# Kernel optimization log

Hardware: AMD Instinct MI355X
Metric: run time of the kernel (lower is better)

Reference implementation:

```python
import jax, jax.numpy as jnp
import numpy as np

B, Z, A, H = 2048, 64, 8, 512

def setup_inputs() -> dict:
    key = jax.random.key(0)
    ks = jax.random.split(key, 7)
    s = 1.0 / np.sqrt(H).astype(np.float32)
    z = jax.random.normal(ks[0], (B, Z), jnp.float32)
    # PyTorch LSTM params, gate order [i, f, g, o]
    W_ih = jax.random.uniform(ks[1], (4 * H, A + Z), jnp.float32, -s, s)
    W_hh = jax.random.uniform(ks[2], (4 * H, H), jnp.float32, -s, s)
    b_ih = jax.random.uniform(ks[3], (4 * H,), jnp.float32, -s, s)
    b_hh = jax.random.uniform(ks[4], (4 * H,), jnp.float32, -s, s)
    W_out = jax.random.uniform(ks[5], (A, H), jnp.float32, -s, s)
    b_out = jax.random.uniform(ks[6], (A,), jnp.float32, -s, s)
    return {"z": z, "W_ih": W_ih, "W_hh": W_hh, "b_ih": b_ih, "b_hh": b_hh,
            "W_out": W_out, "b_out": b_out, "seq_len": 64}


def reference(z, W_ih, W_hh, b_ih, b_hh, W_out, b_out, seq_len):
    batch = z.shape[0]
    hidden = W_hh.shape[1]
    act = W_out.shape[0]
    # dec_in_t = [zeros_a, z] is identical at every timestep -> hoist input proj
    dec_in = jnp.concatenate([jnp.zeros((batch, act), z.dtype), z], axis=-1)
    x_proj = dec_in @ W_ih.T + b_ih + b_hh  # (B, 4H), constant per step

    def step(carry, _):
        h, c = carry
        gates = x_proj + h @ W_hh.T  # (B, 4H)
        i, f, g, o = jnp.split(gates, 4, axis=-1)
        i = jax.nn.sigmoid(i)
        f = jax.nn.sigmoid(f)
        g = jnp.tanh(g)
        o = jax.nn.sigmoid(o)
        c = f * c + i * g
        h = o * jnp.tanh(c)
        return (h, c), h

    init = (jnp.zeros((batch, hidden), z.dtype), jnp.zeros((batch, hidden), z.dtype))
    _, hs = jax.lax.scan(step, init, None, length=seq_len)  # (T, B, H)
    hs = jnp.transpose(hs, (1, 0, 2))  # (B, T, H)
    return hs @ W_out.T + b_out  # (B, T, A)
```

## Files before the change

kernel.cpp:

```cpp
#include <hip/hip_runtime.h>


#define HID   512
#define TSTEP 64
#define KCAT  576

typedef __attribute__((ext_vector_type(8))) short bf16x8;
typedef __attribute__((ext_vector_type(4))) float f32x4;

__device__ inline unsigned short f2bf(float f) {
  unsigned int u = __builtin_bit_cast(unsigned int, f);
  unsigned int r = (u + 0x7fffu + ((u >> 16) & 1u)) >> 16;
  return (unsigned short)r;
}
__device__ inline float sigm(float x) { return 1.0f / (1.0f + __expf(-x)); }
__device__ inline float tanh_f(float x) { return 1.0f - 2.0f / (__expf(2.0f * x) + 1.0f); }

__device__ inline void gl16(const unsigned short* g, unsigned short* l) {
  __builtin_amdgcn_global_load_lds(
      (const __attribute__((address_space(1))) unsigned int*)g,
      (__attribute__((address_space(3))) unsigned int*)l, 16, 0, 0);
}

__global__ void k_prep(const float* __restrict__ z, const float* __restrict__ wih,
                       const float* __restrict__ whh, const float* __restrict__ bih,
                       const float* __restrict__ bhh,
                       unsigned short* __restrict__ wcat, unsigned short* __restrict__ zbf,
                       float* __restrict__ bias) {
  int c = blockIdx.x * 256 + threadIdx.x;
  if (c < 147456) {
    int n = c / 72, kc = (c % 72) * 8;
    unsigned short u[8];
#pragma unroll
    for (int e = 0; e < 8; ++e) {
      int k = kc + e;
      float v = (k < 512) ? whh[(size_t)n * 512 + k] : wih[(size_t)n * 72 + 8 + (k - 512)];
      u[e] = f2bf(v);
    }
    *(bf16x8*)&wcat[(size_t)n * KCAT + kc] = *(bf16x8*)u;
  } else if (c < 163840) {
    int i = c - 147456;
    int row = i >> 3, kc = (i & 7) * 8;
    unsigned short u[8];
#pragma unroll
    for (int e = 0; e < 8; ++e) u[e] = f2bf(z[(size_t)row * 64 + kc + e]);
    *(bf16x8*)&zbf[(size_t)row * 64 + kc] = *(bf16x8*)u;
  } else if (c < 165888) {
    int n = c - 163840;
    bias[n] = bih[n] + bhh[n];
  }
}

template <int GATES, int PROJ>
__global__ __launch_bounds__(256, 2) void k_step(
    const unsigned short* __restrict__ hprev, unsigned short* __restrict__ hnext,
    const unsigned short* __restrict__ wcat, const unsigned short* __restrict__ zbf,
    const float* __restrict__ wout, const float* __restrict__ bias,
    const float* __restrict__ bout, float* __restrict__ cst,
    float* __restrict__ out, int t) {
  __shared__ unsigned short Ab[2][64 * 64];
  __shared__ unsigned short Bb[2][128 * 64];
  __shared__ unsigned short wo_lds[16 * 512];
  __shared__ unsigned short hO[64 * 40];

  const int bid = blockIdx.x;
  const int nt = GATES ? (((bid & 7) << 1) | ((bid >> 8) & 1)) : 0;
  const int bt = GATES ? ((bid >> 3) & 31) : bid;
  const int tid = threadIdx.x;
  const int lane = tid & 63;
  const int wv = tid >> 6;
  const int mq = wv >> 1, nh = wv & 1;
  const int cl = lane & 15, q8 = lane >> 4;
  const int b0 = bt * 64, j0 = nt * 32;

  const int rA = tid >> 3;
  const int xA = ((tid & 7) ^ (rA & 7)) * 8;
  const unsigned short* srcA0 = hprev + (size_t)(b0 + rA) * HID + xA;
  const unsigned short* srcA1 = hprev + (size_t)(b0 + 32 + rA) * HID + xA;
  const unsigned short* srcZ0 = zbf + (size_t)(b0 + rA) * 64 + xA;
  const unsigned short* srcZ1 = zbf + (size_t)(b0 + 32 + rA) * 64 + xA;
  const unsigned short* srcB[4];
#pragma unroll
  for (int k = 0; k < 4; ++k) {
    int rB = k * 32 + rA;
    int n = (rB >> 5) * HID + j0 + (rB & 31);
    srcB[k] = wcat + (size_t)n * KCAT + xA;
  }

  auto do_stage = [&](int buf, int kkv) {
    if (GATES) {
      if (kkv == 8) {
        gl16(srcZ0, &Ab[buf][(wv * 64) * 8]);
        gl16(srcZ1, &Ab[buf][(256 + wv * 64) * 8]);
      } else {
        gl16(srcA0 + kkv * 64, &Ab[buf][(wv * 64) * 8]);
        gl16(srcA1 + kkv * 64, &Ab[buf][(256 + wv * 64) * 8]);
      }
#pragma unroll
      for (int k = 0; k < 4; ++k)
        gl16(srcB[k] + kkv * 64, &Bb[buf][(k * 256 + wv * 64) * 8]);
    } else {
      gl16(srcA0 + kkv * 64, &Ab[buf][(wv * 64) * 8]);
      gl16(srcA1 + kkv * 64, &Ab[buf][(256 + wv * 64) * 8]);
    }
  };

  if (PROJ) {
    int r = tid >> 4, s0 = tid & 15;
#pragma unroll
    for (int i = 0; i < 4; ++i) {
      int s = s0 + i * 16;
      unsigned short u[8] = {0, 0, 0, 0, 0, 0, 0, 0};
      if (r < 8) {
        const float* wp = wout + (size_t)r * 512 + s * 8;
        float4 f0 = *(const float4*)wp;
        float4 f1 = *(const float4*)(wp + 4);
        u[0] = f2bf(f0.x); u[1] = f2bf(f0.y); u[2] = f2bf(f0.z); u[3] = f2bf(f0.w);
        u[4] = f2bf(f1.x); u[5] = f2bf(f1.y); u[6] = f2bf(f1.z); u[7] = f2bf(f1.w);
      }
      int off = r * 512 + (s >> 3) * 64 + (((s & 7) ^ (r & 7)) * 8);
      *(bf16x8*)&wo_lds[off] = *(bf16x8*)u;
    }
  }

  f32x4 acc[4][2];
  if (GATES) {
#pragma unroll
    for (int g = 0; g < 4; ++g) {
      float bv = bias[g * HID + j0 + nh * 16 + cl];
      f32x4 v = {bv, bv, bv, bv};
      acc[g][0] = v; acc[g][1] = v;
    }
  }
  f32x4 accp0 = {0, 0, 0, 0}, accp1 = {0, 0, 0, 0};
  if (PROJ) {
    float bo = (cl < 8) ? bout[cl] : 0.0f;
    f32x4 v = {bo, bo, bo, bo};
    accp0 = v; accp1 = v;
  }

  const size_t cbase = ((size_t)bid * 256 + tid) * 8;
  f32x4 c0 = {0, 0, 0, 0}, c1 = {0, 0, 0, 0};
  if (GATES && t > 0) { c0 = *(const f32x4*)&cst[cbase]; c1 = *(const f32x4*)&cst[cbase + 4]; }

  auto mfma_block = [&](int bu, int kkv) {
    const unsigned short* Al = Ab[bu];
    const unsigned short* Bl = Bb[bu];
#pragma unroll
    for (int ks = 0; ks < 2; ++ks) {
      const int sx = ((ks * 4 + q8) ^ (cl & 7)) * 8;
      bf16x8 af0 = *(const bf16x8*)&Al[(mq * 32 + cl) * 64 + sx];
      bf16x8 af1 = *(const bf16x8*)&Al[(mq * 32 + 16 + cl) * 64 + sx];
      if (GATES) {
#pragma unroll
        for (int g = 0; g < 4; ++g) {
          bf16x8 bf = *(const bf16x8*)&Bl[(g * 32 + nh * 16 + cl) * 64 + sx];
          acc[g][0] = __builtin_amdgcn_mfma_f32_16x16x32_bf16(af0, bf, acc[g][0], 0, 0, 0);
          acc[g][1] = __builtin_amdgcn_mfma_f32_16x16x32_bf16(af1, bf, acc[g][1], 0, 0, 0);
        }
      }
      if (PROJ && nh == 0 && kkv < 8) {
        bf16x8 wf = *(const bf16x8*)&wo_lds[cl * 512 + kkv * 64 + sx];
        accp0 = __builtin_amdgcn_mfma_f32_16x16x32_bf16(af0, wf, accp0, 0, 0, 0);
        accp1 = __builtin_amdgcn_mfma_f32_16x16x32_bf16(af1, wf, accp1, 0, 0, 0);
      }
    }
  };

#define MEMBAR() asm volatile("" ::: "memory")
#define HWBAR()  __builtin_amdgcn_s_barrier()

  if (GATES && t == 0) {
    do_stage(0, 8);
    asm volatile("s_waitcnt vmcnt(0) lgkmcnt(0)" ::: "memory");
    HWBAR(); MEMBAR();
    mfma_block(0, 8);
  } else {
    do_stage(0, 0);
    do_stage(1, 1);
    if (GATES) asm volatile("s_waitcnt vmcnt(6) lgkmcnt(0)" ::: "memory");
    else       asm volatile("s_waitcnt vmcnt(2) lgkmcnt(0)" ::: "memory");
    HWBAR(); MEMBAR();
    const int kkEnd = GATES ? 8 : 7;
    for (int kk = 0;; ++kk) {
      mfma_block(kk & 1, kk);
      if (kk == kkEnd) break;
      MEMBAR(); HWBAR(); MEMBAR();
      if (kk + 2 <= kkEnd) {
        do_stage(kk & 1, kk + 2);
        if (GATES) asm volatile("s_waitcnt vmcnt(6)" ::: "memory");
        else       asm volatile("s_waitcnt vmcnt(2)" ::: "memory");
      } else {
        asm volatile("s_waitcnt vmcnt(0)" ::: "memory");
      }
      MEMBAR(); HWBAR(); MEMBAR();
    }
  }

  if (PROJ && nh == 0 && cl < 8) {
    const int tt = t - 1;
#pragma unroll
    for (int r = 0; r < 4; ++r) {
      int b = b0 + mq * 32 + q8 * 4 + r;
      out[((size_t)b * 64 + tt) * 8 + cl] = accp0[r];
      out[((size_t)(b + 16) * 64 + tt) * 8 + cl] = accp1[r];
    }
  }

  if (GATES) {
#pragma unroll
    for (int fm = 0; fm < 2; ++fm) {
      f32x4 cold = fm ? c1 : c0;
      f32x4 cn;
#pragma unroll
      for (int r = 0; r < 4; ++r) {
        float iv = sigm(acc[0][fm][r]);
        float fv = sigm(acc[1][fm][r]);
        float gv = tanh_f(acc[2][fm][r]);
        float ov = sigm(acc[3][fm][r]);
        float cv = fv * cold[r] + iv * gv;
        cn[r] = cv;
        hO[(mq * 32 + fm * 16 + q8 * 4 + r) * 40 + nh * 16 + cl] = f2bf(ov * tanh_f(cv));
      }
      if (fm) c1 = cn; else c0 = cn;
    }
    *(f32x4*)&cst[cbase] = c0;
    *(f32x4*)&cst[cbase + 4] = c1;
    __syncthreads();

    int row = tid >> 2, sg4 = tid & 3;
    unsigned short tmp[8];
#pragma unroll
    for (int e = 0; e < 8; ++e) tmp[e] = hO[row * 40 + sg4 * 8 + e];
    *(int4*)&hnext[(size_t)(b0 + row) * HID + j0 + sg4 * 8] = *(int4*)tmp;
  }
#undef MEMBAR
#undef HWBAR
}

extern "C" void kernel_launch(void* const* d_in, const int* in_sizes, int n_in,
                              void* d_out, int out_size, void* d_ws, size_t ws_size,
                              hipStream_t stream) {
  const float* z    = (const float*)d_in[0];
  const float* wih  = (const float*)d_in[1];
  const float* whh  = (const float*)d_in[2];
  const float* bih  = (const float*)d_in[3];
  const float* bhh  = (const float*)d_in[4];
  const float* wout = (const float*)d_in[5];
  const float* bout = (const float*)d_in[6];
  float* out = (float*)d_out;

  char* ws = (char*)d_ws;
  unsigned short* wcat = (unsigned short*)(ws);
  unsigned short* zbf  = (unsigned short*)(ws + 2359296);
  float* bias          = (float*)(ws + 2621440);
  unsigned short* h0   = (unsigned short*)(ws + 2629632);
  unsigned short* h1   = (unsigned short*)(ws + 4726784);
  float* cst           = (float*)(ws + 6823936);

  k_prep<<<dim3(648), dim3(256), 0, stream>>>(z, wih, whh, bih, bhh, wcat, zbf, bias);

  for (int t = 0; t < TSTEP; ++t) {
    const unsigned short* hp = (t & 1) ? h0 : h1;
    unsigned short* hn = (t & 1) ? h1 : h0;
    if (t == 0)
      k_step<1, 0><<<dim3(512), dim3(256), 0, stream>>>(hp, hn, wcat, zbf, wout, bias,
                                                        bout, cst, out, t);
    else
      k_step<1, 1><<<dim3(512), dim3(256), 0, stream>>>(hp, hn, wcat, zbf, wout, bias,
                                                        bout, cst, out, t);
  }
  k_step<0, 1><<<dim3(32), dim3(256), 0, stream>>>(h1, h0, wcat, zbf, wout, bias,
                                                   bout, cst, out, TSTEP);
}
```

Baseline: 926.7 us.

## Replace per-timestep launches with persistent cooperative kernel using flag-based sync

Replaces the 65 per-timestep kernel launches with one cooperative persistent kernel of 512 blocks. Each block keeps its cell state in registers across steps, keeps the z tile and W_out in LDS, and waits on per-batch-tile counters in global memory before reading the previous h. The aim is to remove launch overhead and the c-state round-trip through global memory. The cost is spin-wait latency and a reliance on all 512 blocks being co-resident; if the cooperative launch fails, the old multi-launch path runs instead.

```diff
diff --git a/kernel.cpp b/kernel.cpp
--- a/kernel.cpp
+++ b/kernel.cpp
@@ -5,6 +5,7 @@
 #define TSTEP 64
 #define KCAT  576
 
+typedef unsigned long long u64;
 typedef __attribute__((ext_vector_type(8))) short bf16x8;
 typedef __attribute__((ext_vector_type(4))) float f32x4;
 
@@ -51,8 +52,269 @@
   }
 }
 
+__global__ void k_zero(int* __restrict__ flags) {
+  int g = blockIdx.x * 256 + threadIdx.x;
+  if (g < TSTEP * 32) flags[g] = 0;
+}
+
+struct P {
+  const unsigned short *wcat, *zbf;
+  const float *bias, *wout, *bout;
+  unsigned short *h0, *h1;
+  float* out;
+  int* flags;
+};
+
+#define ATOMLD(PTR) __hip_atomic_load((PTR), __ATOMIC_RELAXED, __HIP_MEMORY_SCOPE_AGENT)
+#define ATOMST(PTR, V) __hip_atomic_store((PTR), (V), __ATOMIC_RELAXED, __HIP_MEMORY_SCOPE_AGENT)
+
+#define SMEM_SZ 78848
+
+__global__ __launch_bounds__(256, 2) void k_persist(P p) {
+  extern __shared__ char smem[];
+  unsigned short* Bb[2] = {(unsigned short*)smem, (unsigned short*)(smem + 16384)};
+  unsigned short* Ab[2] = {(unsigned short*)(smem + 32768), (unsigned short*)(smem + 40960)};
+  unsigned short* zA    = (unsigned short*)(smem + 49152);
+  unsigned short* wo    = (unsigned short*)(smem + 57344);
+  unsigned short* hO    = (unsigned short*)(smem + 73728);
+
+  const int bid = blockIdx.x;
+  const int nt = bid >> 5, bt = bid & 31;
+  const int tid = threadIdx.x;
+  const int lane = tid & 63;
+  const int wv = tid >> 6;
+  const int mq = wv >> 1, nh = wv & 1;
+  const int cl = lane & 15, q8 = lane >> 4;
+  const int b0 = bt * 64, j0 = nt * 32;
+
+  const int rS = tid >> 3;
+  const int xS = ((tid & 7) ^ (rS & 7)) * 8;
+  const unsigned short* srcB[4];
+#pragma unroll
+  for (int k = 0; k < 4; ++k) {
+    int rB = k * 32 + rS;
+    int n = (rB >> 5) * HID + j0 + (rB & 31);
+    srcB[k] = p.wcat + (size_t)n * KCAT + xS;
+  }
+#define STAGEB(BUF, CHUNK) { _Pragma("unroll") for (int k4 = 0; k4 < 4; ++k4) \
+    gl16(srcB[k4] + (CHUNK) * 64, &Bb[BUF][(k4 * 256 + wv * 64) * 8]); }
+
+  const int arow = tid >> 2, aseg = tid & 3;
+  const int aoff0 = arow * 64 + (((aseg * 2 + 0) ^ (arow & 7)) * 8);
+  const int aoff1 = arow * 64 + (((aseg * 2 + 1) ^ (arow & 7)) * 8);
+#define AWRITE(DST, R) do { \
+    *(u64*)&(DST)[aoff0] = (R)[0]; *(u64*)&(DST)[aoff0 + 4] = (R)[1]; \
+    *(u64*)&(DST)[aoff1] = (R)[2]; *(u64*)&(DST)[aoff1 + 4] = (R)[3]; } while (0)
+
+  {
+    const u64* zp = (const u64*)(p.zbf + (size_t)(b0 + arow) * 64) + aseg * 4;
+    u64 zr[4] = {zp[0], zp[1], zp[2], zp[3]};
+    AWRITE(zA, zr);
+  }
+  if (nt == 0) {
+    int r = tid >> 4, s0 = tid & 15;
+#pragma unroll
+    for (int i = 0; i < 4; ++i) {
+      int s = s0 + i * 16;
+      unsigned short u[8] = {0, 0, 0, 0, 0, 0, 0, 0};
+      if (r < 8) {
+        const float* wp = p.wout + (size_t)r * 512 + s * 8;
+        float4 f0 = *(const float4*)wp;
+        float4 f1 = *(const float4*)(wp + 4);
+        u[0] = f2bf(f0.x); u[1] = f2bf(f0.y); u[2] = f2bf(f0.z); u[3] = f2bf(f0.w);
+        u[4] = f2bf(f1.x); u[5] = f2bf(f1.y); u[6] = f2bf(f1.z); u[7] = f2bf(f1.w);
+      }
+      int off = r * 512 + (s >> 3) * 64 + (((s & 7) ^ (r & 7)) * 8);
+      *(bf16x8*)&wo[off] = *(bf16x8*)u;
+    }
+  }
+
+  float bias_r[4];
+#pragma unroll
+  for (int g = 0; g < 4; ++g) bias_r[g] = p.bias[g * HID + j0 + nh * 16 + cl];
+  f32x4 c0 = {0, 0, 0, 0}, c1 = {0, 0, 0, 0};
+  f32x4 acc[4][2];
+  f32x4 accp0, accp1;
+  const float boutv = (cl < 8) ? p.bout[cl] : 0.0f;
+
+  auto mfma_block = [&](const unsigned short* Al, const unsigned short* Bl,
+                        int kkv, bool doProj) {
+#pragma unroll
+    for (int ks = 0; ks < 2; ++ks) {
+      const int sx = ((ks * 4 + q8) ^ (cl & 7)) * 8;
+      bf16x8 af0 = *(const bf16x8*)&Al[(mq * 32 + cl) * 64 + sx];
+      bf16x8 af1 = *(const bf16x8*)&Al[(mq * 32 + 16 + cl) * 64 + sx];
+#pragma unroll
+      for (int g = 0; g < 4; ++g) {
+        bf16x8 bf = *(const bf16x8*)&Bl[(g * 32 + nh * 16 + cl) * 64 + sx];
+        acc[g][0] = __builtin_amdgcn_mfma_f32_16x16x32_bf16(af0, bf, acc[g][0], 0, 0, 0);
+        acc[g][1] = __builtin_amdgcn_mfma_f32_16x16x32_bf16(af1, bf, acc[g][1], 0, 0, 0);
+      }
+      if (doProj && nh == 0 && kkv < 8) {
+        bf16x8 wf = *(const bf16x8*)&wo[cl * 512 + kkv * 64 + sx];
+        accp0 = __builtin_amdgcn_mfma_f32_16x16x32_bf16(af0, wf, accp0, 0, 0, 0);
+        accp1 = __builtin_amdgcn_mfma_f32_16x16x32_bf16(af1, wf, accp1, 0, 0, 0);
+      }
+    }
+  };
+
+  auto cell_and_store = [&](unsigned short* hcur, int t) {
+#pragma unroll
+    for (int fm = 0; fm < 2; ++fm) {
+      f32x4 cold = fm ? c1 : c0;
+      f32x4 cn;
+#pragma unroll
+      for (int r = 0; r < 4; ++r) {
+        float iv = sigm(acc[0][fm][r]);
+        float fv = sigm(acc[1][fm][r]);
+        float gv = tanh_f(acc[2][fm][r]);
+        float ov = sigm(acc[3][fm][r]);
+        float cv = fv * cold[r] + iv * gv;
+        cn[r] = cv;
+        hO[(mq * 32 + fm * 16 + q8 * 4 + r) * 40 + nh * 16 + cl] = f2bf(ov * tanh_f(cv));
+      }
+      if (fm) c1 = cn; else c0 = cn;
+    }
+    __syncthreads();
+    u64 u0 = *(const u64*)&hO[arow * 40 + aseg * 8];
+    u64 u1 = *(const u64*)&hO[arow * 40 + aseg * 8 + 4];
+    u64* dst = (u64*)(hcur + (size_t)(b0 + arow) * HID + j0 + aseg * 8);
+    ATOMST(dst, u0);
+    ATOMST(dst + 1, u1);
+    asm volatile("s_waitcnt vmcnt(0)" ::: "memory");
+    __syncthreads();
+    if (tid == 0)
+      __hip_atomic_fetch_add(&p.flags[t * 32 + bt], 1, __ATOMIC_RELAXED,
+                             __HIP_MEMORY_SCOPE_AGENT);
+  };
+
+#define SPIN(IDX) do { if (tid == 0) { \
+      while (__hip_atomic_load(&p.flags[IDX], __ATOMIC_RELAXED, \
+                               __HIP_MEMORY_SCOPE_AGENT) < 16) \
+        __builtin_amdgcn_s_sleep(2); } __syncthreads(); } while (0)
+#define MEMBAR() asm volatile("" ::: "memory")
+#define HWBAR()  __builtin_amdgcn_s_barrier()
+
+  STAGEB(0, 8);
+  asm volatile("s_waitcnt vmcnt(0) lgkmcnt(0)" ::: "memory");
+  HWBAR(); MEMBAR();
+#pragma unroll
+  for (int g = 0; g < 4; ++g) {
+    f32x4 v = {bias_r[g], bias_r[g], bias_r[g], bias_r[g]};
+    acc[g][0] = v; acc[g][1] = v;
+  }
+  mfma_block(zA, Bb[0], 8, false);
+  MEMBAR(); HWBAR(); MEMBAR();
+  cell_and_store(p.h0, 0);
+
+  for (int t = 1; t < TSTEP; ++t) {
+    const unsigned short* hprev = (t & 1) ? p.h0 : p.h1;
+    unsigned short* hcur = (t & 1) ? p.h1 : p.h0;
+    SPIN((t - 1) * 32 + bt);
+
+    const u64* hrow = (const u64*)(hprev + (size_t)(b0 + arow) * HID);
+    u64 ra[2][4];
+#pragma unroll
+    for (int i = 0; i < 4; ++i) ra[0][i] = ATOMLD(hrow + 0 * 16 + aseg * 4 + i);
+    STAGEB(0, 0);
+#pragma unroll
+    for (int i = 0; i < 4; ++i) ra[1][i] = ATOMLD(hrow + 1 * 16 + aseg * 4 + i);
+    STAGEB(1, 1);
+    AWRITE(Ab[0], ra[0]);
+    asm volatile("s_waitcnt vmcnt(8) lgkmcnt(0)" ::: "memory");
+    HWBAR(); MEMBAR();
+
+#pragma unroll
+    for (int g = 0; g < 4; ++g) {
+      f32x4 v = {bias_r[g], bias_r[g], bias_r[g], bias_r[g]};
+      acc[g][0] = v; acc[g][1] = v;
+    }
+    {
+      f32x4 v = {boutv, boutv, boutv, boutv};
+      accp0 = v; accp1 = v;
+    }
+
+#pragma unroll
+    for (int kk = 0; kk <= 8; ++kk) {
+      mfma_block(kk < 8 ? Ab[kk & 1] : zA, Bb[kk & 1], kk, (nt == 0));
+      if (kk == 8) break;
+      MEMBAR(); HWBAR(); MEMBAR();
+      if (kk + 2 <= 7) {
+        AWRITE(Ab[(kk + 1) & 1], ra[(kk + 1) & 1]);
+#pragma unroll
+        for (int i = 0; i < 4; ++i)
+          ra[kk & 1][i] = ATOMLD(hrow + (kk + 2) * 16 + aseg * 4 + i);
+        STAGEB(kk & 1, kk + 2);
+        asm volatile("s_waitcnt vmcnt(8) lgkmcnt(0)" ::: "memory");
+      } else if (kk + 2 == 8) {
+        AWRITE(Ab[(kk + 1) & 1], ra[(kk + 1) & 1]);
+        STAGEB(kk & 1, 8);
+        asm volatile("s_waitcnt vmcnt(4) lgkmcnt(0)" ::: "memory");
+      } else {
+        asm volatile("s_waitcnt vmcnt(0) lgkmcnt(0)" ::: "memory");
+      }
+      MEMBAR(); HWBAR(); MEMBAR();
+    }
+
+    if (nt == 0 && nh == 0 && cl < 8) {
+      const int tt = t - 1;
+#pragma unroll
+      for (int r = 0; r < 4; ++r) {
+        int b = b0 + mq * 32 + q8 * 4 + r;
+        p.out[((size_t)b * 64 + tt) * 8 + cl] = accp0[r];
+        p.out[((size_t)(b + 16) * 64 + tt) * 8 + cl] = accp1[r];
+      }
+    }
+    cell_and_store(hcur, t);
+  }
+
+  if (nt == 0) {
+    SPIN(63 * 32 + bt);
+    const u64* hrow = (const u64*)(p.h1 + (size_t)(b0 + arow) * HID);
+    u64 rr[32];
+#pragma unroll
+    for (int kk = 0; kk < 8; ++kk)
+#pragma unroll
+      for (int i = 0; i < 4; ++i)
+        rr[kk * 4 + i] = ATOMLD(hrow + kk * 16 + aseg * 4 + i);
+    f32x4 ap0 = {boutv, boutv, boutv, boutv};
+    f32x4 ap1 = ap0;
+#pragma unroll
+    for (int kk = 0; kk < 8; ++kk) {
+      AWRITE(Ab[0], (&rr[kk * 4]));
+      asm volatile("s_waitcnt lgkmcnt(0)" ::: "memory");
+      HWBAR(); MEMBAR();
+#pragma unroll
+      for (int ks = 0; ks < 2; ++ks) {
+        const int sx = ((ks * 4 + q8) ^ (cl & 7)) * 8;
+        bf16x8 af0 = *(const bf16x8*)&Ab[0][(mq * 32 + cl) * 64 + sx];
+        bf16x8 af1 = *(const bf16x8*)&Ab[0][(mq * 32 + 16 + cl) * 64 + sx];
+        if (nh == 0) {
+          bf16x8 wf = *(const bf16x8*)&wo[cl * 512 + kk * 64 + sx];
+          ap0 = __builtin_amdgcn_mfma_f32_16x16x32_bf16(af0, wf, ap0, 0, 0, 0);
+          ap1 = __builtin_amdgcn_mfma_f32_16x16x32_bf16(af1, wf, ap1, 0, 0, 0);
+        }
+      }
+      MEMBAR(); HWBAR(); MEMBAR();
+    }
+    if (nh == 0 && cl < 8) {
+#pragma unroll
+      for (int r = 0; r < 4; ++r) {
+        int b = b0 + mq * 32 + q8 * 4 + r;
+        p.out[((size_t)b * 64 + 63) * 8 + cl] = ap0[r];
+        p.out[((size_t)(b + 16) * 64 + 63) * 8 + cl] = ap1[r];
+      }
+    }
+  }
+#undef STAGEB
+#undef AWRITE
+#undef SPIN
+#undef MEMBAR
+#undef HWBAR
+}
+
 template <int GATES, int PROJ>
-__global__ __launch_bounds__(256, 2) void k_step(
+__global__ __launch_bounds__(256, 2) void k_stepF(
     const unsigned short* __restrict__ hprev, unsigned short* __restrict__ hnext,
     const unsigned short* __restrict__ wcat, const unsigned short* __restrict__ zbf,
     const float* __restrict__ wout, const float* __restrict__ bias,
@@ -167,25 +429,24 @@
     }
   };
 
-#define MEMBAR() asm volatile("" ::: "memory")
-#define HWBAR()  __builtin_amdgcn_s_barrier()
-
+#define MEMBARF() asm volatile("" ::: "memory")
+#define HWBARF()  __builtin_amdgcn_s_barrier()
   if (GATES && t == 0) {
     do_stage(0, 8);
     asm volatile("s_waitcnt vmcnt(0) lgkmcnt(0)" ::: "memory");
-    HWBAR(); MEMBAR();
+    HWBARF(); MEMBARF();
     mfma_block(0, 8);
   } else {
     do_stage(0, 0);
     do_stage(1, 1);
     if (GATES) asm volatile("s_waitcnt vmcnt(6) lgkmcnt(0)" ::: "memory");
     else       asm volatile("s_waitcnt vmcnt(2) lgkmcnt(0)" ::: "memory");
-    HWBAR(); MEMBAR();
+    HWBARF(); MEMBARF();
     const int kkEnd = GATES ? 8 : 7;
     for (int kk = 0;; ++kk) {
       mfma_block(kk & 1, kk);
       if (kk == kkEnd) break;
-      MEMBAR(); HWBAR(); MEMBAR();
+      MEMBARF(); HWBARF(); MEMBARF();
       if (kk + 2 <= kkEnd) {
         do_stage(kk & 1, kk + 2);
         if (GATES) asm volatile("s_waitcnt vmcnt(6)" ::: "memory");
@@ -193,7 +454,7 @@
       } else {
         asm volatile("s_waitcnt vmcnt(0)" ::: "memory");
       }
-      MEMBAR(); HWBAR(); MEMBAR();
+      MEMBARF(); HWBARF(); MEMBARF();
     }
   }
 
@@ -227,15 +488,14 @@
     *(f32x4*)&cst[cbase] = c0;
     *(f32x4*)&cst[cbase + 4] = c1;
     __syncthreads();
-
     int row = tid >> 2, sg4 = tid & 3;
     unsigned short tmp[8];
 #pragma unroll
     for (int e = 0; e < 8; ++e) tmp[e] = hO[row * 40 + sg4 * 8 + e];
     *(int4*)&hnext[(size_t)(b0 + row) * HID + j0 + sg4 * 8] = *(int4*)tmp;
   }
-#undef MEMBAR
-#undef HWBAR
+#undef MEMBARF
+#undef HWBARF
 }
 
 extern "C" void kernel_launch(void* const* d_in, const int* in_sizes, int n_in,
@@ -256,20 +516,33 @@
   float* bias          = (float*)(ws + 2621440);
   unsigned short* h0   = (unsigned short*)(ws + 2629632);
   unsigned short* h1   = (unsigned short*)(ws + 4726784);
-  float* cst           = (float*)(ws + 6823936);
+  int* flags           = (int*)(ws + 6823936);
+  float* cst           = (float*)(ws + 6832128);
 
   k_prep<<<dim3(648), dim3(256), 0, stream>>>(z, wih, whh, bih, bhh, wcat, zbf, bias);
+  k_zero<<<dim3(8), dim3(256), 0, stream>>>(flags);
+
+  P pp;
+  pp.wcat = wcat; pp.zbf = zbf; pp.bias = bias; pp.wout = wout; pp.bout = bout;
+  pp.h0 = h0; pp.h1 = h1; pp.out = out; pp.flags = flags;
+
+  hipFuncSetAttribute((const void*)k_persist,
+                      hipFuncAttributeMaxDynamicSharedMemorySize, SMEM_SZ);
+  void* args[] = {&pp};
+  hipError_t e = hipLaunchCooperativeKernel((const void*)k_persist, dim3(512), dim3(256),
+                                            args, SMEM_SZ, stream);
+  if (e == hipSuccess) return;
 
   for (int t = 0; t < TSTEP; ++t) {
     const unsigned short* hp = (t & 1) ? h0 : h1;
     unsigned short* hn = (t & 1) ? h1 : h0;
     if (t == 0)
-      k_step<1, 0><<<dim3(512), dim3(256), 0, stream>>>(hp, hn, wcat, zbf, wout, bias,
-                                                        bout, cst, out, t);
+      k_stepF<1, 0><<<dim3(512), dim3(256), 0, stream>>>(hp, hn, wcat, zbf, wout, bias,
+                                                         bout, cst, out, t);
     else
-      k_step<1, 1><<<dim3(512), dim3(256), 0, stream>>>(hp, hn, wcat, zbf, wout, bias,
-                                                        bout, cst, out, t);
-  }
-  k_step<0, 1><<<dim3(32), dim3(256), 0, stream>>>(h1, h0, wcat, zbf, wout, bias,
-                                                   bout, cst, out, TSTEP);
-}
+      k_stepF<1, 1><<<dim3(512), dim3(256), 0, stream>>>(hp, hn, wcat, zbf, wout, bias,
+                                                         bout, cst, out, t);
+  }
+  k_stepF<0, 1><<<dim3(32), dim3(256), 0, stream>>>(h1, h0, wcat, zbf, wout, bias,
+                                                    bout, cst, out, TSTEP);
+}
```

Result: slower. 1.064 ms (+14.8%).
